# Kernel optimization log

Hardware: AMD Instinct MI355X
Metric: run time of the kernel (lower is better)

## Reference

```python
import jax, jax.numpy as jnp
import numpy as np

B, N, G, E = 4, 8192, 512, 512
D = 3 * E  # fused channel dim = 1536
BN_EPS = 1e-5


def setup_inputs() -> dict:
    key = jax.random.key(0)
    ks = jax.random.split(key, 8)
    f32 = jnp.float32
    return {
        "xyz": jax.random.normal(ks[0], (B, N, 3), f32),
        "centers": jax.random.normal(ks[1], (B, G, 3), f32),
        "H4": jax.random.normal(ks[2], (B, G, E), f32),
        "H8": jax.random.normal(ks[3], (B, G, E), f32),
        "H12": jax.random.normal(ks[4], (B, G, E), f32),
        "w1": jax.random.normal(ks[5], (512, D), f32) * 0.02,
        "b1": jnp.zeros((512,), f32),
        "g1": jnp.ones((512,), f32),
        "be1": jnp.zeros((512,), f32),
        "m1": jnp.zeros((512,), f32),
        "v1": jnp.ones((512,), f32),
        "w2": jax.random.normal(ks[6], (512, 512), f32) * 0.02,
        "b2": jnp.zeros((512,), f32),
        "g2": jnp.ones((512,), f32),
        "be2": jnp.zeros((512,), f32),
        "m2": jnp.zeros((512,), f32),
        "v2": jnp.ones((512,), f32),
    }


def _bn(x, gamma, beta, mean, var):
    # BatchNorm1d, eval mode with running stats (per-channel, last axis)
    return (x - mean) * jax.lax.rsqrt(var + BN_EPS) * gamma + beta


def reference(xyz, centers, H4, H8, H12,
              w1, b1, g1, be1, m1, v1,
              w2, b2, g2, be2, m2, v2):
    fused = jnp.concatenate([H4, H8, H12], axis=-1)  # [B,G,D]
    # squared pairwise distances [B,N,G]
    d = (jnp.sum(xyz * xyz, axis=-1, keepdims=True)
         + jnp.sum(centers * centers, axis=-1)[:, None, :]
         - 2.0 * jnp.einsum('bnc,bgc->bng', xyz, centers))
    neg_d3, idx = jax.lax.top_k(-d, 3)  # 3 smallest distances, ascending
    d3 = -neg_d3  # [B,N,3]
    recip = 1.0 / (d3 + 1e-8)
    w = recip / jnp.sum(recip, axis=-1, keepdims=True)  # [B,N,3]
    # gather neighbor features: [B,N,3,D]
    gathered = jax.vmap(lambda f, i: f[i])(fused, idx)
    interp = jnp.einsum('bnk,bnkd->bnd', w, gathered)  # [B,N,D]
    # 1x1 conv == per-point linear; conv -> BN(eval) -> ReLU, twice
    h = jax.nn.relu(_bn(interp @ w1.T + b1, g1, be1, m1, v1))
    h = jax.nn.relu(_bn(h @ w2.T + b2, g2, be2, m2, v2))
    return h  # [B,N,512]
```

## Files before the change

### kernel.cpp

```cpp
#include <hip/hip_runtime.h>
#include <hip/hip_cooperative_groups.h>
#include <stdint.h>

#define NP 8192
#define NG 512
#define DF 1536

namespace cg = cooperative_groups;

using f32x4    = __attribute__((ext_vector_type(4))) float;
using bf16x8   = __attribute__((ext_vector_type(8))) __bf16;
using ushort8v = __attribute__((ext_vector_type(8))) unsigned short;


__device__ __forceinline__ unsigned short f32_to_bf16(float f) {
  unsigned int u = __float_as_uint(f);
  u += 0x7fffu + ((u >> 16) & 1u);
  return (unsigned short)(u >> 16);
}
__device__ __forceinline__ float bf2f(unsigned short u) {
  return __uint_as_float(((unsigned)u) << 16);
}

struct FusedArgs {
  const float *xyz, *centers, *H4, *H8, *H12, *w1, *w2;
  const float *g1, *be1, *m1, *v1, *g2, *be2, *m2, *v2, *b1, *b2;
  unsigned short *fswz, *w1s, *w2s, *Amatb;
  int *nidx; float *nw, *s1, *t1, *s2, *t2;
  float *outp;
};

__device__ void phase_setup(const FusedArgs& a, char* smem, int w) {
  const int tid = threadIdx.x;
  if (w < 512) {
    float4* cs = (float4*)smem;
    const int b = w >> 7;
    for (int i = tid; i < NG; i += 256) {
      float c0 = a.centers[((size_t)b * NG + i) * 3 + 0];
      float c1 = a.centers[((size_t)b * NG + i) * 3 + 1];
      float c2 = a.centers[((size_t)b * NG + i) * 3 + 2];
      float4 v; v.x = c0; v.y = c1; v.z = c2; v.w = c0 * c0 + c1 * c1 + c2 * c2;
      cs[(i >> 7) * 129 + (i & 127)] = v;
    }
    __syncthreads();
    const int t = (w & 127) * 256 + tid;
    const int p = t >> 2, q = t & 3;
    const size_t pi = (size_t)b * NP + p;
    const float x0 = a.xyz[pi * 3 + 0], x1 = a.xyz[pi * 3 + 1], x2 = a.xyz[pi * 3 + 2];
    const float xx = x0 * x0 + x1 * x1 + x2 * x2;
    float d0 = 3.4e38f, d1 = 3.4e38f, d2 = 3.4e38f;
    int i0 = 0, i1 = 0, i2 = 0;
    const int gbase = q * 128;
    const float4* csq = cs + q * 129;
#pragma unroll 4
    for (int j = 0; j < 128; ++j) {
      float4 c = csq[j];
      float d = xx + c.w - 2.0f * (x0 * c.x + x1 * c.y + x2 * c.z);
      int g = gbase + j;
      bool c0 = d < d0, c1 = d < d1, c2 = d < d2;
      float nd2 = c1 ? d1 : (c2 ? d : d2); int ni2 = c1 ? i1 : (c2 ? g : i2);
      float nd1 = c0 ? d0 : (c1 ? d : d1); int ni1 = c0 ? i0 : (c1 ? g : i1);
      d0 = c0 ? d : d0;                    i0 = c0 ? g : i0;
      d1 = nd1; i1 = ni1; d2 = nd2; i2 = ni2;
    }
#pragma unroll
    for (int off = 1; off <= 2; off <<= 1) {
      float e0 = __shfl_xor(d0, off), e1 = __shfl_xor(d1, off), e2 = __shfl_xor(d2, off);
      int j0 = __shfl_xor(i0, off), j1 = __shfl_xor(i1, off), j2 = __shfl_xor(i2, off);
#pragma unroll
      for (int s = 0; s < 3; ++s) {
        float e = (s == 0) ? e0 : (s == 1 ? e1 : e2);
        int   j = (s == 0) ? j0 : (s == 1 ? j1 : j2);
        bool c0 = (e < d0) || (e == d0 && j < i0);
        bool c1 = (e < d1) || (e == d1 && j < i1);
        bool c2 = (e < d2) || (e == d2 && j < i2);
        float nd2 = c1 ? d1 : (c2 ? e : d2); int ni2 = c1 ? i1 : (c2 ? j : i2);
        float nd1 = c0 ? d0 : (c1 ? e : d1); int ni1 = c0 ? i0 : (c1 ? j : i1);
        d0 = c0 ? e : d0;                    i0 = c0 ? j : i0;
        d1 = nd1; i1 = ni1; d2 = nd2; i2 = ni2;
      }
    }
    if (q == 0) {
      float r0 = 1.0f / (d0 + 1e-8f), r1 = 1.0f / (d1 + 1e-8f), r2 = 1.0f / (d2 + 1e-8f);
      float inv = 1.0f / (r0 + r1 + r2);
      a.nw[pi * 3 + 0] = r0 * inv; a.nw[pi * 3 + 1] = r1 * inv; a.nw[pi * 3 + 2] = r2 * inv;
      a.nidx[pi * 3 + 0] = i0; a.nidx[pi * 3 + 1] = i1; a.nidx[pi * 3 + 2] = i2;
    }
    __syncthreads();
  } else if (w < 2048) {
    const int qd = (w - 512) * 256 + tid;
    const int L = qd & 63, t2 = qd >> 6;
    const int kc = t2 % 48, mg = t2 / 48;
    const int m = mg * 16 + (L & 15);
    const int k = kc * 32 + (L >> 4) * 8;
    const float* src = (k < 512) ? a.H4 : (k < 1024 ? a.H8 : a.H12);
    const float* sp = &src[(size_t)m * 512 + (k & 511)];
    float4 va = *(const float4*)sp, vb = *(const float4*)(sp + 4);
    ushort8v o;
    o[0] = f32_to_bf16(va.x); o[1] = f32_to_bf16(va.y);
    o[2] = f32_to_bf16(va.z); o[3] = f32_to_bf16(va.w);
    o[4] = f32_to_bf16(vb.x); o[5] = f32_to_bf16(vb.y);
    o[6] = f32_to_bf16(vb.z); o[7] = f32_to_bf16(vb.w);
    *(ushort8v*)&a.fswz[((size_t)(mg * 48 + kc)) * 512 + L * 8] = o;
  } else if (w < 2432) {
    const int qd = (w - 2048) * 256 + tid;
    const int L = qd & 63, t2 = qd >> 6;
    const int kc = t2 % 48, ng = t2 / 48;
    const int n = ng * 16 + (L & 15);
    const int k = kc * 32 + (L >> 4) * 8;
    const float* sp = &a.w1[(size_t)n * 1536 + k];
    float4 va = *(const float4*)sp, vb = *(const float4*)(sp + 4);
    ushort8v o;
    o[0] = f32_to_bf16(va.x); o[1] = f32_to_bf16(va.y);
    o[2] = f32_to_bf16(va.z); o[3] = f32_to_bf16(va.w);
    o[4] = f32_to_bf16(vb.x); o[5] = f32_to_bf16(vb.y);
    o[6] = f32_to_bf16(vb.z); o[7] = f32_to_bf16(vb.w);
    *(ushort8v*)&a.w1s[((size_t)(ng * 48 + kc)) * 512 + L * 8] = o;
  } else if (w < 2560) {
    const int qd = (w - 2432) * 256 + tid;
    const int L = qd & 63, t2 = qd >> 6;
    const int kc = t2 & 15, ng = t2 >> 4;
    const int n = ng * 16 + (L & 15);
    const int k = kc * 32 + (L >> 4) * 8;
    const float* sp = &a.w2[(size_t)n * 512 + k];
    float4 va = *(const float4*)sp, vb = *(const float4*)(sp + 4);
    ushort8v o;
    o[0] = f32_to_bf16(va.x); o[1] = f32_to_bf16(va.y);
    o[2] = f32_to_bf16(va.z); o[3] = f32_to_bf16(va.w);
    o[4] = f32_to_bf16(vb.x); o[5] = f32_to_bf16(vb.y);
    o[6] = f32_to_bf16(vb.z); o[7] = f32_to_bf16(vb.w);
    *(ushort8v*)&a.w2s[((size_t)(ng * 16 + kc)) * 512 + L * 8] = o;
  } else {
    for (int i = tid; i < 512; i += 256) {
      float sa = a.g1[i] / sqrtf(a.v1[i] + 1e-5f);
      a.s1[i] = sa; a.t1[i] = a.be1[i] - a.m1[i] * sa;
      float sb = a.g2[i] / sqrtf(a.v2[i] + 1e-5f);
      a.s2[i] = sb; a.t2[i] = a.be2[i] - a.m2[i] * sb;
    }
  }
}

__device__ void phase_gemm1(const FusedArgs& a, char* smem) {
  float* red = (float*)smem;
  const int tid = threadIdx.x, lane = tid & 63, wv = tid >> 6;
  const int blk = blockIdx.x;
  const int m0 = (blk >> 3) * 32;
  const int n0 = (blk & 7) * 64;
  const unsigned short* Ap = a.fswz + ((size_t)(m0 >> 4) * 48 + wv * 12) * 512 + lane * 8;
  const unsigned short* Bp = a.w1s  + ((size_t)(n0 >> 4) * 48 + wv * 12) * 512 + lane * 8;

  f32x4 acc[2][4];
#pragma unroll
  for (int i = 0; i < 2; ++i)
#pragma unroll
    for (int j = 0; j < 4; ++j) acc[i][j] = (f32x4){0.f, 0.f, 0.f, 0.f};

  bf16x8 af[2], bfr[4], afn[2], bfn[4];
#pragma unroll
  for (int i = 0; i < 2; ++i)
    af[i]  = __builtin_bit_cast(bf16x8, *(const ushort8v*)(Ap + (size_t)i * 48 * 512));
#pragma unroll
  for (int i = 0; i < 4; ++i)
    bfr[i] = __builtin_bit_cast(bf16x8, *(const ushort8v*)(Bp + (size_t)i * 48 * 512));
#pragma unroll 1
  for (int kc = 0; kc < 12; ++kc) {
    if (kc < 11) {
#pragma unroll
      for (int i = 0; i < 2; ++i)
        afn[i] = __builtin_bit_cast(bf16x8, *(const ushort8v*)(Ap + (size_t)i * 48 * 512 + (kc + 1) * 512));
#pragma unroll
      for (int i = 0; i < 4; ++i)
        bfn[i] = __builtin_bit_cast(bf16x8, *(const ushort8v*)(Bp + (size_t)i * 48 * 512 + (kc + 1) * 512));
    }
#pragma unroll
    for (int mi = 0; mi < 2; ++mi)
#pragma unroll
      for (int ni = 0; ni < 4; ++ni)
        acc[mi][ni] = __builtin_amdgcn_mfma_f32_16x16x32_bf16(af[mi], bfr[ni], acc[mi][ni], 0, 0, 0);
#pragma unroll
    for (int i = 0; i < 2; ++i) af[i] = afn[i];
#pragma unroll
    for (int i = 0; i < 4; ++i) bfr[i] = bfn[i];
  }

  for (int w = 0; w < 4; ++w) {
    if (wv == w) {
#pragma unroll
      for (int mi = 0; mi < 2; ++mi)
#pragma unroll
        for (int ni = 0; ni < 4; ++ni) {
          int col = ni * 16 + (lane & 15);
#pragma unroll
          for (int r = 0; r < 4; ++r) {
            int row = mi * 16 + (lane >> 4) * 4 + r;
            if (w == 0) red[row * 65 + col] = acc[mi][ni][r];
            else        red[row * 65 + col] += acc[mi][ni][r];
          }
        }
    }
    __syncthreads();
  }
  const int row = tid >> 3;
  const int col = (tid & 7) * 8;
  ushort8v o;
#pragma unroll
  for (int j = 0; j < 8; ++j) {
    int n = n0 + col + j;
    float v = red[row * 65 + col + j];
    o[j] = f32_to_bf16(a.s1[n] * (v + a.b1[n]) + a.t1[n]);
  }
  *(ushort8v*)&a.Amatb[(size_t)(m0 + row) * 512 + n0 + col] = o;
  __syncthreads();
}

__device__ void phase_mega(const FusedArgs& a, char* smem) {
  unsigned short* hl = (unsigned short*)smem;
  const int tid = threadIdx.x, lane = tid & 63, wv = tid >> 6;
  const int xcd = blockIdx.x & 7, slot = blockIdx.x >> 3;
  const int m0 = (xcd * 64 + slot) * 64;

  {
    const int p = m0 + wv * 16 + (lane & 15);
    const int b = p >> 13;
    const int i0 = a.nidx[p * 3 + 0], i1 = a.nidx[p * 3 + 1], i2 = a.nidx[p * 3 + 2];
    const float w0 = a.nw[p * 3 + 0], w1v = a.nw[p * 3 + 1], w2v = a.nw[p * 3 + 2];
    const int co = (lane >> 4) * 8;
    const unsigned short* A0 = a.Amatb + ((size_t)(b * 512 + i0)) * 512 + co;
    const unsigned short* A1 = a.Amatb + ((size_t)(b * 512 + i1)) * 512 + co;
    const unsigned short* A2 = a.Amatb + ((size_t)(b * 512 + i2)) * 512 + co;
    unsigned short* wp = hl + (size_t)(wv * 16) * 512 + lane * 8;
#pragma unroll 4
    for (int kc = 0; kc < 16; ++kc) {
      ushort8v u0 = *(const ushort8v*)(A0 + kc * 32);
      ushort8v u1 = *(const ushort8v*)(A1 + kc * 32);
      ushort8v u2 = *(const ushort8v*)(A2 + kc * 32);
      ushort8v o;
#pragma unroll
      for (int j = 0; j < 8; ++j) {
        float v = w0 * bf2f(u0[j]) + w1v * bf2f(u1[j]) + w2v * bf2f(u2[j]);
        o[j] = f32_to_bf16(fmaxf(v, 0.f));
      }
      *(ushort8v*)(wp + (size_t)kc * 512) = o;
    }
  }
  __syncthreads();

  const int n0 = wv * 128;
  const unsigned short* Bbase = a.w2s + (size_t)(n0 >> 4) * 16 * 512 + lane * 8;

  f32x4 acc[4][8];
#pragma unroll
  for (int i = 0; i < 4; ++i)
#pragma unroll
    for (int j = 0; j < 8; ++j) acc[i][j] = (f32x4){0.f, 0.f, 0.f, 0.f};

#pragma unroll 1
  for (int kc = 0; kc < 16; ++kc) {
    bf16x8 af[4], bfr[8];
#pragma unroll
    for (int mi = 0; mi < 4; ++mi)
      af[mi] = __builtin_bit_cast(bf16x8,
          *(const ushort8v*)(hl + (size_t)(mi * 16 + kc) * 512 + lane * 8));
#pragma unroll
    for (int ni = 0; ni < 8; ++ni)
      bfr[ni] = __builtin_bit_cast(bf16x8,
          *(const ushort8v*)(Bbase + (size_t)(ni * 16 + kc) * 512));
#pragma unroll
    for (int mi = 0; mi < 4; ++mi)
#pragma unroll
      for (int ni = 0; ni < 8; ++ni)
        acc[mi][ni] = __builtin_amdgcn_mfma_f32_16x16x32_bf16(af[mi], bfr[ni], acc[mi][ni], 0, 0, 0);
  }

#pragma unroll
  for (int mi = 0; mi < 4; ++mi) {
    int mbase = m0 + mi * 16 + (lane >> 4) * 4;
#pragma unroll
    for (int ni = 0; ni < 8; ++ni) {
      int n = n0 + ni * 16 + (lane & 15);
      float s = a.s2[n], bb = a.b2[n], t = a.t2[n];
      f32x4 v = acc[mi][ni];
#pragma unroll
      for (int r = 0; r < 4; ++r)
        a.outp[(size_t)(mbase + r) * 512 + n] = fmaxf(s * (v[r] + bb) + t, 0.f);
    }
  }
}

__global__ __launch_bounds__(256, 2) void fused_kernel(FusedArgs a) {
  __shared__ __align__(16) char smem[65536];
  cg::grid_group grid = cg::this_grid();
  const int blk = blockIdx.x;
  for (int u = blk; u <= 2560; u += 512) phase_setup(a, smem, u);
  grid.sync();
  phase_gemm1(a, smem);
  grid.sync();
  phase_mega(a, smem);
}

__global__ __launch_bounds__(256) void k_setup(FusedArgs a) {
  __shared__ __align__(16) char smem[8448];
  for (int u = blockIdx.x; u <= 2560; u += 512) phase_setup(a, smem, u);
}
__global__ __launch_bounds__(256) void k_gemm1(FusedArgs a) {
  __shared__ __align__(16) char smem[8448];
  phase_gemm1(a, smem);
}
__global__ __launch_bounds__(256, 2) void k_mega(FusedArgs a) {
  __shared__ __align__(16) char smem[65536];
  phase_mega(a, smem);
}

extern "C" void kernel_launch(void* const* d_in, const int* in_sizes, int n_in,
                              void* d_out, int out_size, void* d_ws, size_t ws_size,
                              hipStream_t stream) {
  char* ws = (char*)d_ws;
  FusedArgs a;
  a.xyz     = (const float*)d_in[0];
  a.centers = (const float*)d_in[1];
  a.H4      = (const float*)d_in[2];
  a.H8      = (const float*)d_in[3];
  a.H12     = (const float*)d_in[4];
  a.w1      = (const float*)d_in[5];
  a.b1      = (const float*)d_in[6];
  a.g1      = (const float*)d_in[7];
  a.be1     = (const float*)d_in[8];
  a.m1      = (const float*)d_in[9];
  a.v1      = (const float*)d_in[10];
  a.w2      = (const float*)d_in[11];
  a.b2      = (const float*)d_in[12];
  a.g2      = (const float*)d_in[13];
  a.be2     = (const float*)d_in[14];
  a.m2      = (const float*)d_in[15];
  a.v2      = (const float*)d_in[16];
  a.fswz  = (unsigned short*)(ws);
  a.w1s   = (unsigned short*)(ws + 6291456);
  a.w2s   = (unsigned short*)(ws + 7864320);
  a.Amatb = (unsigned short*)(ws + 8388608);
  a.nidx  = (int*)           (ws + 10485760);
  a.nw    = (float*)         (ws + 10878976);
  a.s1    = (float*)         (ws + 11272192);
  a.t1 = a.s1 + 512; a.s2 = a.t1 + 512; a.t2 = a.s2 + 512;
  a.outp  = (float*)d_out;

  int nb = 0;
  hipError_t qerr = hipOccupancyMaxActiveBlocksPerMultiprocessor(
      &nb, reinterpret_cast<const void*>(fused_kernel), 256, 0);
  bool coop_ok = (qerr == hipSuccess) && (nb >= 2);
  if (coop_ok) {
    void* kp[] = { (void*)&a };
    hipError_t lerr = hipLaunchCooperativeKernel(
        (const void*)fused_kernel, dim3(512), dim3(256), kp, 0, stream);
    coop_ok = (lerr == hipSuccess);
  }
  if (!coop_ok) {
    k_setup <<<512, 256, 0, stream>>>(a);
    k_gemm1 <<<512, 256, 0, stream>>>(a);
    k_mega  <<<512, 256, 0, stream>>>(a);
  }
}
```

Measured before the change: 166.8 us.

## Double grid to 1024 blocks with halved tiles and 4 blocks per CU

Grid goes from 512 to 1024 cooperative blocks. GEMM1 tiles shrink to 32x32 and mega tiles to 32 rows, with shared memory cut to 32KB so four blocks fit per CU. The gather-interpolate step now splits each 16-row group's K range across two waves, and output stores become nontemporal. The aim is more parallelism and latency hiding across the grid syncs, at the cost of more reloads of weight tiles per output element and less reuse per block.

```diff
diff --git a/kernel.cpp b/kernel.cpp
--- a/kernel.cpp
+++ b/kernel.cpp
@@ -144,43 +144,39 @@
   float* red = (float*)smem;
   const int tid = threadIdx.x, lane = tid & 63, wv = tid >> 6;
   const int blk = blockIdx.x;
-  const int m0 = (blk >> 3) * 32;
-  const int n0 = (blk & 7) * 64;
+  const int m0 = (blk >> 4) * 32;
+  const int n0 = (blk & 15) * 32;
   const unsigned short* Ap = a.fswz + ((size_t)(m0 >> 4) * 48 + wv * 12) * 512 + lane * 8;
   const unsigned short* Bp = a.w1s  + ((size_t)(n0 >> 4) * 48 + wv * 12) * 512 + lane * 8;
 
-  f32x4 acc[2][4];
+  f32x4 acc[2][2];
 #pragma unroll
   for (int i = 0; i < 2; ++i)
 #pragma unroll
-    for (int j = 0; j < 4; ++j) acc[i][j] = (f32x4){0.f, 0.f, 0.f, 0.f};
-
-  bf16x8 af[2], bfr[4], afn[2], bfn[4];
-#pragma unroll
-  for (int i = 0; i < 2; ++i)
+    for (int j = 0; j < 2; ++j) acc[i][j] = (f32x4){0.f, 0.f, 0.f, 0.f};
+
+  bf16x8 af[2], bfr[2], afn[2], bfn[2];
+#pragma unroll
+  for (int i = 0; i < 2; ++i) {
     af[i]  = __builtin_bit_cast(bf16x8, *(const ushort8v*)(Ap + (size_t)i * 48 * 512));
-#pragma unroll
-  for (int i = 0; i < 4; ++i)
     bfr[i] = __builtin_bit_cast(bf16x8, *(const ushort8v*)(Bp + (size_t)i * 48 * 512));
+  }
 #pragma unroll 1
   for (int kc = 0; kc < 12; ++kc) {
     if (kc < 11) {
 #pragma unroll
-      for (int i = 0; i < 2; ++i)
+      for (int i = 0; i < 2; ++i) {
         afn[i] = __builtin_bit_cast(bf16x8, *(const ushort8v*)(Ap + (size_t)i * 48 * 512 + (kc + 1) * 512));
-#pragma unroll
-      for (int i = 0; i < 4; ++i)
         bfn[i] = __builtin_bit_cast(bf16x8, *(const ushort8v*)(Bp + (size_t)i * 48 * 512 + (kc + 1) * 512));
+      }
     }
 #pragma unroll
     for (int mi = 0; mi < 2; ++mi)
 #pragma unroll
-      for (int ni = 0; ni < 4; ++ni)
+      for (int ni = 0; ni < 2; ++ni)
         acc[mi][ni] = __builtin_amdgcn_mfma_f32_16x16x32_bf16(af[mi], bfr[ni], acc[mi][ni], 0, 0, 0);
 #pragma unroll
-    for (int i = 0; i < 2; ++i) af[i] = afn[i];
-#pragma unroll
-    for (int i = 0; i < 4; ++i) bfr[i] = bfn[i];
+    for (int i = 0; i < 2; ++i) { af[i] = afn[i]; bfr[i] = bfn[i]; }
   }
 
   for (int w = 0; w < 4; ++w) {
@@ -188,28 +184,29 @@
 #pragma unroll
       for (int mi = 0; mi < 2; ++mi)
 #pragma unroll
-        for (int ni = 0; ni < 4; ++ni) {
+        for (int ni = 0; ni < 2; ++ni) {
           int col = ni * 16 + (lane & 15);
 #pragma unroll
           for (int r = 0; r < 4; ++r) {
             int row = mi * 16 + (lane >> 4) * 4 + r;
-            if (w == 0) red[row * 65 + col] = acc[mi][ni][r];
-            else        red[row * 65 + col] += acc[mi][ni][r];
+            if (w == 0) red[row * 33 + col] = acc[mi][ni][r];
+            else        red[row * 33 + col] += acc[mi][ni][r];
           }
         }
     }
     __syncthreads();
   }
   const int row = tid >> 3;
-  const int col = (tid & 7) * 8;
-  ushort8v o;
-#pragma unroll
-  for (int j = 0; j < 8; ++j) {
-    int n = n0 + col + j;
-    float v = red[row * 65 + col + j];
-    o[j] = f32_to_bf16(a.s1[n] * (v + a.b1[n]) + a.t1[n]);
-  }
-  *(ushort8v*)&a.Amatb[(size_t)(m0 + row) * 512 + n0 + col] = o;
+  const int col = (tid & 7) * 4;
+  ushort4 o;
+  float v0 = red[row * 33 + col + 0], v1 = red[row * 33 + col + 1];
+  float v2 = red[row * 33 + col + 2], v3 = red[row * 33 + col + 3];
+  int n = n0 + col;
+  o.x = f32_to_bf16(a.s1[n + 0] * (v0 + a.b1[n + 0]) + a.t1[n + 0]);
+  o.y = f32_to_bf16(a.s1[n + 1] * (v1 + a.b1[n + 1]) + a.t1[n + 1]);
+  o.z = f32_to_bf16(a.s1[n + 2] * (v2 + a.b1[n + 2]) + a.t1[n + 2]);
+  o.w = f32_to_bf16(a.s1[n + 3] * (v3 + a.b1[n + 3]) + a.t1[n + 3]);
+  *(ushort4*)&a.Amatb[(size_t)(m0 + row) * 512 + n] = o;
   __syncthreads();
 }
 
@@ -217,10 +214,11 @@
   unsigned short* hl = (unsigned short*)smem;
   const int tid = threadIdx.x, lane = tid & 63, wv = tid >> 6;
   const int xcd = blockIdx.x & 7, slot = blockIdx.x >> 3;
-  const int m0 = (xcd * 64 + slot) * 64;
+  const int m0 = xcd * 4096 + slot * 32;
 
   {
-    const int p = m0 + wv * 16 + (lane & 15);
+    const int g = wv >> 1, half = wv & 1;
+    const int p = m0 + g * 16 + (lane & 15);
     const int b = p >> 13;
     const int i0 = a.nidx[p * 3 + 0], i1 = a.nidx[p * 3 + 1], i2 = a.nidx[p * 3 + 2];
     const float w0 = a.nw[p * 3 + 0], w1v = a.nw[p * 3 + 1], w2v = a.nw[p * 3 + 2];
@@ -228,9 +226,10 @@
     const unsigned short* A0 = a.Amatb + ((size_t)(b * 512 + i0)) * 512 + co;
     const unsigned short* A1 = a.Amatb + ((size_t)(b * 512 + i1)) * 512 + co;
     const unsigned short* A2 = a.Amatb + ((size_t)(b * 512 + i2)) * 512 + co;
-    unsigned short* wp = hl + (size_t)(wv * 16) * 512 + lane * 8;
-#pragma unroll 4
-    for (int kc = 0; kc < 16; ++kc) {
+    unsigned short* wp = hl + (size_t)g * 16 * 512 + lane * 8;
+#pragma unroll
+    for (int i = 0; i < 8; ++i) {
+      const int kc = half * 8 + i;
       ushort8v u0 = *(const ushort8v*)(A0 + kc * 32);
       ushort8v u1 = *(const ushort8v*)(A1 + kc * 32);
       ushort8v u2 = *(const ushort8v*)(A2 + kc * 32);
@@ -248,32 +247,37 @@
   const int n0 = wv * 128;
   const unsigned short* Bbase = a.w2s + (size_t)(n0 >> 4) * 16 * 512 + lane * 8;
 
-  f32x4 acc[4][8];
-#pragma unroll
-  for (int i = 0; i < 4; ++i)
+  f32x4 acc[2][8];
+#pragma unroll
+  for (int i = 0; i < 2; ++i)
 #pragma unroll
     for (int j = 0; j < 8; ++j) acc[i][j] = (f32x4){0.f, 0.f, 0.f, 0.f};
 
 #pragma unroll 1
   for (int kc = 0; kc < 16; ++kc) {
-    bf16x8 af[4], bfr[8];
-#pragma unroll
-    for (int mi = 0; mi < 4; ++mi)
-      af[mi] = __builtin_bit_cast(bf16x8,
-          *(const ushort8v*)(hl + (size_t)(mi * 16 + kc) * 512 + lane * 8));
-#pragma unroll
-    for (int ni = 0; ni < 8; ++ni)
-      bfr[ni] = __builtin_bit_cast(bf16x8,
-          *(const ushort8v*)(Bbase + (size_t)(ni * 16 + kc) * 512));
-#pragma unroll
-    for (int mi = 0; mi < 4; ++mi)
-#pragma unroll
-      for (int ni = 0; ni < 8; ++ni)
-        acc[mi][ni] = __builtin_amdgcn_mfma_f32_16x16x32_bf16(af[mi], bfr[ni], acc[mi][ni], 0, 0, 0);
-  }
-
-#pragma unroll
-  for (int mi = 0; mi < 4; ++mi) {
+    bf16x8 af[2];
+#pragma unroll
+    for (int g = 0; g < 2; ++g)
+      af[g] = __builtin_bit_cast(bf16x8,
+          *(const ushort8v*)(hl + (size_t)(g * 16 + kc) * 512 + lane * 8));
+#pragma unroll
+    for (int grp = 0; grp < 2; ++grp) {
+      bf16x8 bfr[4];
+#pragma unroll
+      for (int j = 0; j < 4; ++j)
+        bfr[j] = __builtin_bit_cast(bf16x8,
+            *(const ushort8v*)(Bbase + (size_t)((grp * 4 + j) * 16 + kc) * 512));
+#pragma unroll
+      for (int mi = 0; mi < 2; ++mi)
+#pragma unroll
+        for (int j = 0; j < 4; ++j)
+          acc[mi][grp * 4 + j] = __builtin_amdgcn_mfma_f32_16x16x32_bf16(
+              af[mi], bfr[j], acc[mi][grp * 4 + j], 0, 0, 0);
+    }
+  }
+
+#pragma unroll
+  for (int mi = 0; mi < 2; ++mi) {
     int mbase = m0 + mi * 16 + (lane >> 4) * 4;
 #pragma unroll
     for (int ni = 0; ni < 8; ++ni) {
@@ -282,32 +286,33 @@
       f32x4 v = acc[mi][ni];
 #pragma unroll
       for (int r = 0; r < 4; ++r)
-        a.outp[(size_t)(mbase + r) * 512 + n] = fmaxf(s * (v[r] + bb) + t, 0.f);
-    }
-  }
-}
-
-__global__ __launch_bounds__(256, 2) void fused_kernel(FusedArgs a) {
-  __shared__ __align__(16) char smem[65536];
+        __builtin_nontemporal_store(fmaxf(s * (v[r] + bb) + t, 0.f),
+                                    &a.outp[(size_t)(mbase + r) * 512 + n]);
+    }
+  }
+}
+
+__global__ __launch_bounds__(256, 4) void fused_kernel(FusedArgs a) {
+  __shared__ __align__(16) char smem[32768];
   cg::grid_group grid = cg::this_grid();
   const int blk = blockIdx.x;
-  for (int u = blk; u <= 2560; u += 512) phase_setup(a, smem, u);
+  for (int u = blk; u <= 2560; u += 1024) phase_setup(a, smem, u);
   grid.sync();
   phase_gemm1(a, smem);
   grid.sync();
   phase_mega(a, smem);
 }
 
-__global__ __launch_bounds__(256) void k_setup(FusedArgs a) {
+__global__ __launch_bounds__(256, 4) void k_setup(FusedArgs a) {
   __shared__ __align__(16) char smem[8448];
-  for (int u = blockIdx.x; u <= 2560; u += 512) phase_setup(a, smem, u);
-}
-__global__ __launch_bounds__(256) void k_gemm1(FusedArgs a) {
-  __shared__ __align__(16) char smem[8448];
+  for (int u = blockIdx.x; u <= 2560; u += 1024) phase_setup(a, smem, u);
+}
+__global__ __launch_bounds__(256, 4) void k_gemm1(FusedArgs a) {
+  __shared__ __align__(16) char smem[4224];
   phase_gemm1(a, smem);
 }
-__global__ __launch_bounds__(256, 2) void k_mega(FusedArgs a) {
-  __shared__ __align__(16) char smem[65536];
+__global__ __launch_bounds__(256, 4) void k_mega(FusedArgs a) {
+  __shared__ __align__(16) char smem[32768];
   phase_mega(a, smem);
 }
 
@@ -346,16 +351,16 @@
   int nb = 0;
   hipError_t qerr = hipOccupancyMaxActiveBlocksPerMultiprocessor(
       &nb, reinterpret_cast<const void*>(fused_kernel), 256, 0);
-  bool coop_ok = (qerr == hipSuccess) && (nb >= 2);
+  bool coop_ok = (qerr == hipSuccess) && (nb >= 4);
   if (coop_ok) {
     void* kp[] = { (void*)&a };
     hipError_t lerr = hipLaunchCooperativeKernel(
-        (const void*)fused_kernel, dim3(512), dim3(256), kp, 0, stream);
+        (const void*)fused_kernel, dim3(1024), dim3(256), kp, 0, stream);
     coop_ok = (lerr == hipSuccess);
   }
   if (!coop_ok) {
-    k_setup <<<512, 256, 0, stream>>>(a);
-    k_gemm1 <<<512, 256, 0, stream>>>(a);
-    k_mega  <<<512, 256, 0, stream>>>(a);
-  }
-}
+    k_setup <<<1024, 256, 0, stream>>>(a);
+    k_gemm1 <<<1024, 256, 0, stream>>>(a);
+    k_mega  <<<1024, 256, 0, stream>>>(a);
+  }
+}
```

Result: slower. 176.0 us (+5.5%).
